# Kernel tuning notes

Hardware: AMD Instinct MI355X
Metric: run time of the kernel (lower is better)

The kernel has to match this reference:

```python
import jax, jax.numpy as jnp
import numpy as np
from jax import lax

B = 256
NUM_CLASSES = 10
IN_CAPS = 32 * 6 * 6  # 1152
IN_DIM = 8
OUT_DIM = 16
NUM_ITERS = 3


def squash(t, axis=-1):
    sq = jnp.sum(t * t, axis=axis, keepdims=True)
    return (sq / (1.0 + sq)) * t / jnp.sqrt(sq)


def conv2d(x, w, b, stride):
    y = lax.conv_general_dilated(x, w, (stride, stride), 'VALID',
                                 dimension_numbers=('NCHW', 'OIHW', 'NCHW'))
    return y + b[None, :, None, None]


def setup_inputs() -> dict:
    key = jax.random.key(0)
    ks = jax.random.split(key, 12)
    f = jnp.float32
    return {
        'x': jax.random.uniform(ks[0], (B, 1, 28, 28), dtype=f),
        'conv1_w': jax.random.normal(ks[1], (256, 1, 9, 9), dtype=f) * 0.05,
        'conv1_b': jnp.zeros((256,), dtype=f),
        'prim_w': jax.random.normal(ks[2], (IN_DIM * 32, 256, 9, 9), dtype=f) * 0.02,
        'prim_b': jnp.zeros((IN_DIM * 32,), dtype=f),
        'route_w': jax.random.normal(ks[3], (NUM_CLASSES, IN_CAPS, IN_DIM, OUT_DIM), dtype=f),
        'dec_w1': jax.random.normal(ks[4], (OUT_DIM * NUM_CLASSES, 512), dtype=f) * 0.05,
        'dec_b1': jnp.zeros((512,), dtype=f),
        'dec_w2': jax.random.normal(ks[5], (512, 1024), dtype=f) * 0.04,
        'dec_b2': jnp.zeros((1024,), dtype=f),
        'dec_w3': jax.random.normal(ks[6], (1024, 28 * 28), dtype=f) * 0.03,
        'dec_b3': jnp.zeros((28 * 28,), dtype=f),
    }


def reference(x, conv1_w, conv1_b, prim_w, prim_b, route_w,
              dec_w1, dec_b1, dec_w2, dec_b2, dec_w3, dec_b3):
    bsz = x.shape[0]
    # conv1 + relu -> [B,256,20,20]
    h = jax.nn.relu(conv2d(x, conv1_w, conv1_b, 1))
    # primary capsules: 8 parallel convs (stacked into one) -> [B, 8*32, 6, 6]
    p = conv2d(h, prim_w, prim_b, 2)
    # each capsule conv flattens to [B, 32*36], concatenated along last dim
    p = p.reshape(bsz, IN_DIM, 32 * 6 * 6).transpose(0, 2, 1)  # [B, 1152, 8]
    u = squash(p, axis=-1)
    # priors: [o, b, i, d_out]
    priors = jnp.einsum('bic,oicd->obid', u, route_w)
    # routing by agreement: softmax over in_capsules (dim i), per original code
    logits = jnp.zeros((NUM_CLASSES, bsz, IN_CAPS, 1), dtype=priors.dtype)
    outputs = None
    for it in range(NUM_ITERS):
        probs = jax.nn.softmax(logits, axis=2)              # [o,b,i,1]
        outputs = squash(jnp.sum(probs * priors, axis=2, keepdims=True))  # [o,b,1,d]
        if it != NUM_ITERS - 1:
            logits = logits + jnp.sum(priors * outputs, axis=-1, keepdims=True)
    vecs = outputs.reshape(NUM_CLASSES, bsz, OUT_DIM).transpose(1, 0, 2)  # [B,10,16]
    classes = jnp.sqrt(jnp.sum(vecs * vecs, axis=-1))
    classes = jax.nn.softmax(classes, axis=1)               # [B,10]
    # y=None path: one-hot of predicted class (non-differentiable mask)
    y = jax.nn.one_hot(jnp.argmax(classes, axis=1), NUM_CLASSES, dtype=vecs.dtype)
    dec_in = (vecs * y[:, :, None]).reshape(bsz, -1)        # [B,160]
    hdec = jax.nn.relu(dec_in @ dec_w1 + dec_b1)
    hdec = jax.nn.relu(hdec @ dec_w2 + dec_b2)
    reconstruction = jax.nn.sigmoid(hdec @ dec_w3 + dec_b3)  # [B,784]
    return classes, reconstruction
```

## Files before the change

### kernel.cpp

```cpp
#include <hip/hip_runtime.h>
#include <hip/hip_bf16.h>
#include <math.h>


typedef __attribute__((ext_vector_type(8))) short bf16x8;
typedef __attribute__((ext_vector_type(4))) float f32x4;

__device__ __forceinline__ void gl16(const void* g, void* l) {
  __builtin_amdgcn_global_load_lds((const __attribute__((address_space(1))) void*)g,
                                   (__attribute__((address_space(3))) void*)l,
                                   16, 0, 0);
}

__global__ __launch_bounds__(256) void k_conv1(const float* __restrict__ x,
                                               const float* __restrict__ w,
                                               const float* __restrict__ bias,
                                               __hip_bfloat16* __restrict__ hT) {
  const int bid = blockIdx.x;
  const int img = bid >> 2, ocq = bid & 3;
  __shared__ float xs[784];
  __shared__ float ws[64 * 81];
  __shared__ __attribute__((aligned(16))) __hip_bfloat16 tile[8 * 1288];
  const int t = threadIdx.x;
  const float4* xg = (const float4*)(x + (size_t)img * 784);
  if (t < 196) ((float4*)xs)[t] = xg[t];
  const float4* wg = (const float4*)(w + (size_t)ocq * 64 * 81);
  for (int i = t; i < 1296; i += 256) ((float4*)ws)[i] = wg[i];
  __syncthreads();
  const int ocl = t & 63, rowg = t >> 6;
  const int oc = ocq * 64 + ocl;
  const int chl = ocl >> 3, icl = ocl & 7;
  const float bv = bias[oc];
  __hip_bfloat16* hb = hT + ((size_t)img * 32 + ocq * 8) * 6560;
#pragma unroll 1
  for (int it = 0; it < 5; it++) {
    const int r = it * 4 + rowg;
    float acc[20];
#pragma unroll
    for (int p = 0; p < 20; p++) acc[p] = bv;
#pragma unroll
    for (int ky = 0; ky < 9; ky++) {
      float xr[28];
      const float* xrow = &xs[(r + ky) * 28];
#pragma unroll
      for (int q = 0; q < 7; q++) ((float4*)xr)[q] = ((const float4*)xrow)[q];
      float wr[9];
#pragma unroll
      for (int i = 0; i < 9; i++) wr[i] = ws[ocl * 81 + ky * 9 + i];
#pragma unroll
      for (int kx = 0; kx < 9; kx++)
#pragma unroll
        for (int p = 0; p < 20; p++)
          acc[p] = fmaf(wr[kx], xr[p + kx], acc[p]);
    }
#pragma unroll
    for (int p = 0; p < 20; p++) {
      const float v = fmaxf(acc[p], 0.f);
      const __hip_bfloat16 hi = __float2bfloat16(v);
      const __hip_bfloat16 lo = __float2bfloat16(v - __bfloat162float(hi));
      tile[chl * 1288 + (p * 8 + rowg * 2) * 8 + icl] = hi;
      tile[chl * 1288 + (p * 8 + rowg * 2 + 1) * 8 + icl] = lo;
    }
    __syncthreads();
#pragma unroll
    for (int q = 0; q < 5; q++) {
      const int idx = q * 256 + t;
      const int c2 = idx / 160, rem = idx - c2 * 160;
      const int xx = rem >> 3, j = rem & 7;
      const float4 vdat = *(const float4*)&tile[c2 * 1288 + rem * 8];
      *(float4*)(hb + (size_t)c2 * 6560 + (size_t)(xx * 41 + it * 8 + j) * 8) = vdat;
    }
    __syncthreads();
  }
}

__global__ __launch_bounds__(256) void k_wrep(const float* __restrict__ pw,
                                              __hip_bfloat16* __restrict__ wGp) {
  const int s = blockIdx.x >> 2, ocq = blockIdx.x & 3;
  const int ch = s / 21, tq = s - ch * 21;
  __hip_bfloat16* outp = wGp + ((size_t)s * 4 + ocq) * 4608;
  const int t = threadIdx.x;
  for (int e = t; e < 2048; e += 256) {
    const int ocl = e >> 5, k = e & 31;
    const int tapl = k >> 3, icl = k & 7;
    const int tap = tq * 4 + tapl, ic = ch * 8 + icl;
    const int oc = ocq * 64 + ocl;
    const float v = (tap < 81) ? pw[((size_t)oc * 256 + ic) * 81 + tap] : 0.f;
    const __hip_bfloat16 hi = __float2bfloat16(v);
    const __hip_bfloat16 lo = __float2bfloat16(v - __bfloat162float(hi));
    outp[ocl * 72 + k] = hi;
    outp[ocl * 72 + 32 + k] = lo;
  }
  for (int e = t; e < 512; e += 256) {
    const int ocl = e >> 3, j = e & 7;
    outp[ocl * 72 + 64 + j] = __float2bfloat16(0.f);
  }
}

__global__ __launch_bounds__(256) void k_rrep(const float* __restrict__ rw,
                                              float* __restrict__ rwT) {
  const int o = blockIdx.x / 18, ig = blockIdx.x % 18;
  __shared__ float tile[64 * 129];
  const int t = threadIdx.x;
  for (int idx = t; idx < 64 * 128; idx += 256) {
    const int i = idx >> 7, cd = idx & 127;
    tile[i * 129 + cd] = rw[((size_t)o * 1152 + ig * 64 + i) * 128 + cd];
  }
  __syncthreads();
  for (int idx = t; idx < 64 * 128; idx += 256) {
    const int cd = idx >> 6, il = idx & 63;
    rwT[((size_t)o * 128 + cd) * 1152 + ig * 64 + il] = tile[il * 129 + cd];
  }
}

#define HT_B 52480
#define PQ_F 2359296
__global__ __launch_bounds__(512) void k_conv2(
    const __hip_bfloat16* __restrict__ hTg,
    const __hip_bfloat16* __restrict__ wGp,
    float* __restrict__ pq, int c0) {
  __shared__ char hT[HT_B];
  const int bid = blockIdx.x;
  int ig, ocq, kq;
  if (gridDim.x == 512) {
    ig = (bid & 7) | (((bid >> 5) & 7) << 3);
    ocq = (bid >> 3) & 3;
    kq = bid >> 8;
  } else {
    ig = bid >> 3;
    ocq = (bid >> 1) & 3;
    kq = bid & 1;
  }
  const int t = threadIdx.x;
  const int w = t >> 6, lane = t & 63;
  const int lquad = lane >> 4, lrow = lane & 15;
  const int mhalf = w >> 2;
  const int nt = mhalf ? 4 : 5;
  const int mtb = mhalf ? 5 : 0;
  const int ocg = ocq * 64 + (w & 3) * 16 + lrow;
  int abase[5];
#pragma unroll
  for (int i = 0; i < 5; i++) {
    int m = (mtb + i) * 16 + lrow;
    if (i >= nt) m = 0;
    const int img = m / 36, px = m - img * 36;
    const int oy = px / 6, ox = px - oy * 6;
    abase[i] = img * 13120 + ox * 1312 + oy * 64;
  }
  f32x4 acc[5];
#pragma unroll
  for (int i = 0; i < 5; i++) acc[i] = (f32x4){0.f, 0.f, 0.f, 0.f};

  const char* hgc = (const char*)hTg;
  const char* wp = (const char*)wGp + ((size_t)(kq * 336) * 4 + ocq) * 4608 +
                   ((w & 3) * 16 + lrow) * 144 + lquad * 16;
  bf16x8 bh = *(const bf16x8*)wp;
  bf16x8 bl = *(const bf16x8*)(wp + 64);
  wp += 18432;
#pragma unroll 1
  for (int chl = 0; chl < 16; chl++) {
    const int ch = kq * 16 + chl;
    const char* hch = hgc + ((size_t)(ig * 128) + ch) * 13120;
#pragma unroll
    for (int rr = 0; rr < 6; rr++) {
      const int idx = t + rr * 512;
      const int j = idx / 820, r = idx - j * 820;
      gl16(hch + (size_t)j * 419840 + r * 16, hT + rr * 8192 + w * 1024);
    }
    if (t < 208) {
      const int idx = 3072 + t;
      const int j = idx / 820, r = idx - j * 820;
      gl16(hch + (size_t)j * 419840 + r * 16, hT + 49152 + w * 1024);
    }
    __syncthreads();
#pragma unroll 1
    for (int tq = 0; tq < 21; tq++) {
      const bf16x8 nh = *(const bf16x8*)wp;
      const bf16x8 nl = *(const bf16x8*)(wp + 64);
      wp += 18432;
      const int tt = tq * 4 + lquad;
      const int ky = tt / 9, kx = tt - ky * 9;
      const int toff = kx * 656 + ky * 32;
      bf16x8 ah[5];
#pragma unroll
      for (int i = 0; i < 5; i++)
        ah[i] = *(const bf16x8*)(hT + abase[i] + toff);
#pragma unroll
      for (int i = 0; i < 5; i++)
        if (i < nt) acc[i] = __builtin_amdgcn_mfma_f32_16x16x32_bf16(ah[i], bh, acc[i], 0, 0, 0);
#pragma unroll
      for (int i = 0; i < 5; i++)
        if (i < nt) acc[i] = __builtin_amdgcn_mfma_f32_16x16x32_bf16(ah[i], bl, acc[i], 0, 0, 0);
      bf16x8 al[5];
#pragma unroll
      for (int i = 0; i < 5; i++)
        al[i] = *(const bf16x8*)(hT + abase[i] + toff + 16);
#pragma unroll
      for (int i = 0; i < 5; i++)
        if (i < nt) acc[i] = __builtin_amdgcn_mfma_f32_16x16x32_bf16(al[i], bh, acc[i], 0, 0, 0);
      bh = nh;
      bl = nl;
    }
    __syncthreads();
  }
  float* pblk = pq + (size_t)kq * PQ_F;
#pragma unroll
  for (int i = 0; i < 5; i++) {
    if (i < nt) {
#pragma unroll
      for (int r = 0; r < 4; r++) {
        const int m = (mtb + i) * 16 + lquad * 4 + r;
        const int img = m / 36, px = m - img * 36;
        pblk[((size_t)(c0 + ig * 4 + img) * 36 + px) * 256 + ocg] = acc[i][r];
      }
    }
  }
}

__global__ __launch_bounds__(256) void k_squash(const float* __restrict__ pq,
                                                const float* __restrict__ bias,
                                                float* __restrict__ u) {
  const int gid = blockIdx.x * 256 + threadIdx.x;
  const int b = gid / 1152, i = gid - b * 1152;
  const int cp = i / 36, px = i - cp * 36;
  const float* pb = pq + ((size_t)b * 36 + px) * 256 + cp;
  float s[8];
#pragma unroll
  for (int d = 0; d < 8; d++)
    s[d] = pb[d * 32] + pb[(size_t)PQ_F + d * 32] + bias[cp + d * 32];
  float sq = 0.f;
#pragma unroll
  for (int d = 0; d < 8; d++) sq = fmaf(s[d], s[d], sq);
  const float scale = sq / ((1.f + sq) * sqrtf(sq));
  float o[8];
#pragma unroll
  for (int d = 0; d < 8; d++) o[d] = s[d] * scale;
  float* ub = u + (size_t)gid * 8;
  ((float4*)ub)[0] = ((float4*)o)[0];
  ((float4*)ub)[1] = ((float4*)o)[1];
}

__device__ __forceinline__ float wsum(float v) {
#pragma unroll
  for (int o = 32; o > 0; o >>= 1) v += __shfl_xor(v, o, 64);
  return v;
}
__device__ __forceinline__ float wmaxr(float v) {
#pragma unroll
  for (int o = 32; o > 0; o >>= 1) v = fmaxf(v, __shfl_xor(v, o, 64));
  return v;
}

__global__ __launch_bounds__(512) void k_route(const float* __restrict__ u,
                                               const float* __restrict__ rwT,
                                               float* __restrict__ vecs) {
  const int bid = blockIdx.x;
  int o, b;
  if (bid < 2048) { o = bid & 7; b = bid >> 3; }
  else { const int ix = bid - 2048; o = 8 + (ix & 1); b = ix >> 1; }
  __shared__ __attribute__((aligned(16))) float pri4[4 * 1152 * 4];
  __shared__ float red[8 * 17];
  __shared__ float redm[8];
  const int t = threadIdx.x;
  const int wave = t >> 6, lane = t & 63;
  const float* ub = u + (size_t)b * 9216;
  const float* rwo = rwT + (size_t)o * 128 * 1152;
#pragma unroll
  for (int ci = 0; ci < 3; ci++) {
    const bool valid = (ci < 2) || (t < 128);
    const int i = valid ? (t + ci * 512) : 0;
    float uv[8];
    *(float4*)&uv[0] = *(const float4*)(ub + i * 8);
    *(float4*)&uv[4] = *(const float4*)(ub + i * 8 + 4);
    float a[16];
#pragma unroll
    for (int d = 0; d < 16; d++) a[d] = 0.f;
#pragma unroll
    for (int c = 0; c < 8; c++) {
      const float* wcol = rwo + (size_t)(c * 16) * 1152 + i;
#pragma unroll
      for (int d = 0; d < 16; d++)
        a[d] = fmaf(uv[c], wcol[(size_t)d * 1152], a[d]);
    }
    if (valid) {
#pragma unroll
      for (int q = 0; q < 4; q++)
        *(float4*)&pri4[(q * 1152 + i) * 4] = *(float4*)&a[q * 4];
    }
  }
  __syncthreads();
  float l[3];
#pragma unroll
  for (int ci = 0; ci < 3; ci++)
    l[ci] = ((ci < 2) || (t < 128)) ? 0.f : -1e30f;
  float v[16];
#pragma unroll 1
  for (int it = 0; it < 3; it++) {
    float m = fmaxf(fmaxf(l[0], l[1]), l[2]);
    m = wmaxr(m);
    if (lane == 0) redm[wave] = m;
    __syncthreads();
    m = redm[0];
#pragma unroll
    for (int wv2 = 1; wv2 < 8; wv2++) m = fmaxf(m, redm[wv2]);
    float Z = 0.f, S[16];
#pragma unroll
    for (int d = 0; d < 16; d++) S[d] = 0.f;
#pragma unroll
    for (int ci = 0; ci < 3; ci++) {
      const bool valid = (ci < 2) || (t < 128);
      const int i = valid ? (t + ci * 512) : 0;
      const float e = expf(l[ci] - m);
      Z += e;
#pragma unroll
      for (int q = 0; q < 4; q++) {
        const float4 p4 = *(const float4*)&pri4[(q * 1152 + i) * 4];
        S[q * 4 + 0] = fmaf(e, p4.x, S[q * 4 + 0]);
        S[q * 4 + 1] = fmaf(e, p4.y, S[q * 4 + 1]);
        S[q * 4 + 2] = fmaf(e, p4.z, S[q * 4 + 2]);
        S[q * 4 + 3] = fmaf(e, p4.w, S[q * 4 + 3]);
      }
    }
    Z = wsum(Z);
#pragma unroll
    for (int d = 0; d < 16; d++) S[d] = wsum(S[d]);
    __syncthreads();
    if (lane == 0) {
      red[wave * 17] = Z;
#pragma unroll
      for (int d = 0; d < 16; d++) red[wave * 17 + 1 + d] = S[d];
    }
    __syncthreads();
    float Zt = 0.f;
#pragma unroll
    for (int wv2 = 0; wv2 < 8; wv2++) Zt += red[wv2 * 17];
    float sv[16], sq = 0.f;
#pragma unroll
    for (int d = 0; d < 16; d++) {
      float sd = 0.f;
#pragma unroll
      for (int wv2 = 0; wv2 < 8; wv2++) sd += red[wv2 * 17 + 1 + d];
      sd /= Zt;
      sv[d] = sd;
      sq = fmaf(sd, sd, sq);
    }
    const float scale = sq / ((1.f + sq) * sqrtf(sq));
#pragma unroll
    for (int d = 0; d < 16; d++) v[d] = scale * sv[d];
    if (it < 2) {
#pragma unroll
      for (int ci = 0; ci < 3; ci++) {
        const bool valid = (ci < 2) || (t < 128);
        const int i = valid ? (t + ci * 512) : 0;
        float dot = 0.f;
#pragma unroll
        for (int q = 0; q < 4; q++) {
          const float4 p4 = *(const float4*)&pri4[(q * 1152 + i) * 4];
          dot = fmaf(p4.x, v[q * 4 + 0], dot);
          dot = fmaf(p4.y, v[q * 4 + 1], dot);
          dot = fmaf(p4.z, v[q * 4 + 2], dot);
          dot = fmaf(p4.w, v[q * 4 + 3], dot);
        }
        l[ci] += dot;
      }
      __syncthreads();
    }
  }
  if (t == 0) {
    float* vb = vecs + ((size_t)b * 10 + o) * 16;
#pragma unroll
    for (int d = 0; d < 16; d++) vb[d] = v[d];
  }
}

__global__ __launch_bounds__(64) void k_cls(const float* __restrict__ vecs,
                                            float* __restrict__ out,
                                            float* __restrict__ selvec,
                                            int* __restrict__ amv) {
  const int b = blockIdx.x * 64 + threadIdx.x;
  const float* vb = vecs + (size_t)b * 160;
  float n[10];
#pragma unroll
  for (int o = 0; o < 10; o++) {
    float sq = 0.f;
#pragma unroll
    for (int d = 0; d < 16; d++) { const float xv = vb[o * 16 + d]; sq = fmaf(xv, xv, sq); }
    n[o] = sqrtf(sq);
  }
  float m = n[0];
#pragma unroll
  for (int o = 1; o < 10; o++) m = fmaxf(m, n[o]);
  float e[10], Z = 0.f;
#pragma unroll
  for (int o = 0; o < 10; o++) { e[o] = expf(n[o] - m); Z += e[o]; }
  const float inv = 1.f / Z;
  float cls[10];
#pragma unroll
  for (int o = 0; o < 10; o++) {
    cls[o] = e[o] * inv;
    out[(size_t)b * 10 + o] = cls[o];
  }
  int am = 0;
  float best = cls[0];
#pragma unroll
  for (int o = 1; o < 10; o++)
    if (cls[o] > best) { best = cls[o]; am = o; }
  amv[b] = am;
#pragma unroll
  for (int d = 0; d < 16; d++) selvec[(size_t)b * 16 + d] = vb[am * 16 + d];
}

__global__ __launch_bounds__(512) void k_dec1(const float* __restrict__ selvec,
                                              const int* __restrict__ amv,
                                              const float* __restrict__ w1,
                                              const float* __restrict__ b1,
                                              float* __restrict__ h1) {
  const int b = blockIdx.x, t = threadIdx.x;
  __shared__ float sv[16];
  __shared__ int ams;
  if (t < 16) sv[t] = selvec[(size_t)b * 16 + t];
  if (t == 0) ams = amv[b];
  __syncthreads();
  const float* wrow = w1 + (size_t)ams * 16 * 512;
  float acc = b1[t];
#pragma unroll
  for (int d = 0; d < 16; d++) acc = fmaf(sv[d], wrow[d * 512 + t], acc);
  h1[(size_t)b * 512 + t] = fmaxf(acc, 0.f);
}

__global__ __launch_bounds__(128) void k_dec2(const float* __restrict__ h1,
                                              const float* __restrict__ w2,
                                              const float* __restrict__ b2,
                                              float* __restrict__ h2) {
  const int nc = blockIdx.x >> 5, bg = blockIdx.x & 31;
  const int t = threadIdx.x;
  const int n = nc * 128 + t;
  const int bs = bg * 8;
  __shared__ float h1s[8 * 512];
  __shared__ float wts[32 * 128];
  {
    const float4* src = (const float4*)(h1 + (size_t)bs * 512);
    for (int i = t; i < 1024; i += 128) ((float4*)h1s)[i] = src[i];
  }
  float acc[8];
  const float bb = b2[n];
#pragma unroll
  for (int j = 0; j < 8; j++) acc[j] = bb;
#pragma unroll 1
  for (int kt = 0; kt < 16; kt++) {
    __syncthreads();
#pragma unroll
    for (int r = 0; r < 32; r++)
      wts[r * 128 + t] = w2[(size_t)(kt * 32 + r) * 1024 + n];
    __syncthreads();
#pragma unroll
    for (int k4 = 0; k4 < 8; k4++) {
      float wq[4];
#pragma unroll
      for (int q = 0; q < 4; q++) wq[q] = wts[(k4 * 4 + q) * 128 + t];
#pragma unroll
      for (int j = 0; j < 8; j++) {
        const float4 hv = *(const float4*)&h1s[j * 512 + kt * 32 + k4 * 4];
        acc[j] = fmaf(hv.x, wq[0], acc[j]);
        acc[j] = fmaf(hv.y, wq[1], acc[j]);
        acc[j] = fmaf(hv.z, wq[2], acc[j]);
        acc[j] = fmaf(hv.w, wq[3], acc[j]);
      }
    }
  }
#pragma unroll
  for (int j = 0; j < 8; j++) h2[(size_t)(bs + j) * 1024 + n] = fmaxf(acc[j], 0.f);
}

__global__ __launch_bounds__(128) void k_dec3(const float* __restrict__ h2,
                                              const float* __restrict__ w3,
                                              const float* __restrict__ b3,
                                              float* __restrict__ out) {
  const int nc = blockIdx.x >> 5, bg = blockIdx.x & 31;
  const int t = threadIdx.x;
  const int bs = bg * 8;
  __shared__ float h2s[8 * 1024];
  __shared__ float wts[32 * 112];
  {
    const float4* src = (const float4*)(h2 + (size_t)bs * 1024);
    for (int i = t; i < 2048; i += 128) ((float4*)h2s)[i] = src[i];
  }
  const int n = nc * 112 + (t < 112 ? t : 0);
  float acc[8];
  const float bb = b3[n];
#pragma unroll
  for (int j = 0; j < 8; j++) acc[j] = bb;
#pragma unroll 1
  for (int kt = 0; kt < 32; kt++) {
    __syncthreads();
#pragma unroll
    for (int r = 0; r < 32; r++)
      if (t < 112) wts[r * 112 + t] = w3[(size_t)(kt * 32 + r) * 784 + n];
    __syncthreads();
    if (t < 112) {
#pragma unroll
      for (int k4 = 0; k4 < 8; k4++) {
        float wq[4];
#pragma unroll
        for (int q = 0; q < 4; q++) wq[q] = wts[(k4 * 4 + q) * 112 + t];
#pragma unroll
        for (int j = 0; j < 8; j++) {
          const float4 hv = *(const float4*)&h2s[j * 1024 + kt * 32 + k4 * 4];
          acc[j] = fmaf(hv.x, wq[0], acc[j]);
          acc[j] = fmaf(hv.y, wq[1], acc[j]);
          acc[j] = fmaf(hv.z, wq[2], acc[j]);
          acc[j] = fmaf(hv.w, wq[3], acc[j]);
        }
      }
    }
  }
  if (t < 112) {
#pragma unroll
    for (int j = 0; j < 8; j++)
      out[(size_t)(bs + j) * 784 + n] = 1.f / (1.f + expf(-acc[j]));
  }
}

extern "C" void kernel_launch(void* const* d_in, const int* in_sizes, int n_in,
                              void* d_out, int out_size, void* d_ws, size_t ws_size,
                              hipStream_t stream) {
  const float* x   = (const float*)d_in[0];
  const float* c1w = (const float*)d_in[1];
  const float* c1b = (const float*)d_in[2];
  const float* pw  = (const float*)d_in[3];
  const float* pb  = (const float*)d_in[4];
  const float* rw  = (const float*)d_in[5];
  const float* w1  = (const float*)d_in[6];
  const float* b1  = (const float*)d_in[7];
  const float* w2  = (const float*)d_in[8];
  const float* b2  = (const float*)d_in[9];
  const float* w3  = (const float*)d_in[10];
  const float* b3  = (const float*)d_in[11];
  float* out = (float*)d_out;
  float* ws = (float*)d_ws;

  const size_t WGP_F = ((size_t)672 * 4 * 4608 + 18432) / 4;
  const size_t U_F = 2359296;
  const size_t RWT_F = 10 * 128 * 1152;
  const size_t SMALL_F = 40960 + 4096 + 256 + 131072 + 262144;
  const size_t fixed_f = WGP_F + 2 * PQ_F + U_F + RWT_F + SMALL_F;
  int chunk = 256;
  while (chunk > 8 && (fixed_f + (size_t)chunk * 104960) * 4 > ws_size) chunk >>= 1;

  __hip_bfloat16* wGp  = (__hip_bfloat16*)ws;
  __hip_bfloat16* hTgc = (__hip_bfloat16*)(ws + WGP_F);
  float* pq   = ws + WGP_F + (size_t)chunk * 104960;
  float* u    = pq + 2 * PQ_F;
  float* rwT  = u + U_F;
  float* vecs = rwT + RWT_F;
  float* sel  = vecs + 40960;
  int*   amv  = (int*)(sel + 4096);
  float* h1   = sel + 4096 + 256;
  float* h2   = h1 + 131072;

  k_wrep<<<dim3(2688), dim3(256), 0, stream>>>(pw, wGp);
  k_rrep<<<dim3(180), dim3(256), 0, stream>>>(rw, rwT);
  for (int c0 = 0; c0 < 256; c0 += chunk) {
    k_conv1<<<dim3(chunk * 4), dim3(256), 0, stream>>>(x + (size_t)c0 * 784, c1w, c1b, hTgc);
    k_conv2<<<dim3((chunk / 4) * 8), dim3(512), 0, stream>>>(hTgc, wGp, pq, c0);
  }
  k_squash<<<dim3(1152), dim3(256), 0, stream>>>(pq, pb, u);
  k_route<<<dim3(2560), dim3(512), 0, stream>>>(u, rwT, vecs);
  k_cls<<<dim3(4), dim3(64), 0, stream>>>(vecs, out, sel, amv);
  k_dec1<<<dim3(256), dim3(512), 0, stream>>>(sel, amv, w1, b1, h1);
  k_dec2<<<dim3(256), dim3(128), 0, stream>>>(h1, w2, b2, h2);
  k_dec3<<<dim3(224), dim3(128), 0, stream>>>(h2, w3, b3, out + 2560);
}
```

Before: 866.0 us.

## Restructure squash, classifier and decoder kernels for coalescing and more blocks

Squash now runs one block per image, staging the summed split-K partial conv outputs through padded shared memory with coalesced float4 loads instead of strided per-thread gathers. The class softmax kernel moves from one thread per image to one block per image, using shared memory for the norms. The decoder GEMM kernels process 2 images per block instead of 8, which quadruples the grid size for better CU occupancy. The cost is that each block re-reads the weight tiles four times as often, raising global weight traffic.

```diff
diff --git a/kernel.cpp b/kernel.cpp
--- a/kernel.cpp
+++ b/kernel.cpp
@@ -220,24 +220,41 @@
 __global__ __launch_bounds__(256) void k_squash(const float* __restrict__ pq,
                                                 const float* __restrict__ bias,
                                                 float* __restrict__ u) {
-  const int gid = blockIdx.x * 256 + threadIdx.x;
-  const int b = gid / 1152, i = gid - b * 1152;
-  const int cp = i / 36, px = i - cp * 36;
-  const float* pb = pq + ((size_t)b * 36 + px) * 256 + cp;
-  float s[8];
-#pragma unroll
-  for (int d = 0; d < 8; d++)
-    s[d] = pb[d * 32] + pb[(size_t)PQ_F + d * 32] + bias[cp + d * 32];
-  float sq = 0.f;
-#pragma unroll
-  for (int d = 0; d < 8; d++) sq = fmaf(s[d], s[d], sq);
-  const float scale = sq / ((1.f + sq) * sqrtf(sq));
-  float o[8];
-#pragma unroll
-  for (int d = 0; d < 8; d++) o[d] = s[d] * scale;
-  float* ub = u + (size_t)gid * 8;
-  ((float4*)ub)[0] = ((float4*)o)[0];
-  ((float4*)ub)[1] = ((float4*)o)[1];
+  const int b = blockIdx.x;
+  __shared__ float ps[36 * 257];
+  const int t = threadIdx.x;
+  const float4* s0 = (const float4*)(pq + (size_t)b * 9216);
+  const float4* s1 = (const float4*)(pq + (size_t)PQ_F + (size_t)b * 9216);
+#pragma unroll
+  for (int q = 0; q < 9; q++) {
+    const int idx = q * 256 + t;
+    const float4 a = s0[idx], c = s1[idx];
+    const int px = idx >> 6, oc = (idx & 63) * 4;
+    float* dst = &ps[px * 257 + oc];
+    dst[0] = a.x + c.x; dst[1] = a.y + c.y;
+    dst[2] = a.z + c.z; dst[3] = a.w + c.w;
+  }
+  __syncthreads();
+#pragma unroll
+  for (int rr = 0; rr < 5; rr++) {
+    const int i = rr * 256 + t;
+    if (i < 1152) {
+      const int cp = i / 36, px = i - cp * 36;
+      float s[8], sq = 0.f;
+#pragma unroll
+      for (int d = 0; d < 8; d++) {
+        s[d] = ps[px * 257 + d * 32 + cp] + bias[d * 32 + cp];
+        sq = fmaf(s[d], s[d], sq);
+      }
+      const float scale = sq / ((1.f + sq) * sqrtf(sq));
+      float o[8];
+#pragma unroll
+      for (int d = 0; d < 8; d++) o[d] = s[d] * scale;
+      float* ub = u + ((size_t)b * 1152 + i) * 8;
+      ((float4*)ub)[0] = ((float4*)o)[0];
+      ((float4*)ub)[1] = ((float4*)o)[1];
+    }
+  }
 }
 
 __device__ __forceinline__ float wsum(float v) {
@@ -377,37 +394,41 @@
                                             float* __restrict__ out,
                                             float* __restrict__ selvec,
                                             int* __restrict__ amv) {
-  const int b = blockIdx.x * 64 + threadIdx.x;
+  const int b = blockIdx.x, t = threadIdx.x;
+  __shared__ float vbs[160];
+  __shared__ float nrm[10];
+  __shared__ int ams;
   const float* vb = vecs + (size_t)b * 160;
-  float n[10];
-#pragma unroll
-  for (int o = 0; o < 10; o++) {
+  for (int idx = t; idx < 160; idx += 64) vbs[idx] = vb[idx];
+  __syncthreads();
+  if (t < 10) {
     float sq = 0.f;
 #pragma unroll
-    for (int d = 0; d < 16; d++) { const float xv = vb[o * 16 + d]; sq = fmaf(xv, xv, sq); }
-    n[o] = sqrtf(sq);
-  }
-  float m = n[0];
-#pragma unroll
-  for (int o = 1; o < 10; o++) m = fmaxf(m, n[o]);
-  float e[10], Z = 0.f;
-#pragma unroll
-  for (int o = 0; o < 10; o++) { e[o] = expf(n[o] - m); Z += e[o]; }
-  const float inv = 1.f / Z;
-  float cls[10];
-#pragma unroll
-  for (int o = 0; o < 10; o++) {
-    cls[o] = e[o] * inv;
-    out[(size_t)b * 10 + o] = cls[o];
-  }
-  int am = 0;
-  float best = cls[0];
-#pragma unroll
-  for (int o = 1; o < 10; o++)
-    if (cls[o] > best) { best = cls[o]; am = o; }
-  amv[b] = am;
-#pragma unroll
-  for (int d = 0; d < 16; d++) selvec[(size_t)b * 16 + d] = vb[am * 16 + d];
+    for (int d = 0; d < 16; d++) { const float xv = vbs[t * 16 + d]; sq = fmaf(xv, xv, sq); }
+    nrm[t] = sqrtf(sq);
+  }
+  __syncthreads();
+  if (t == 0) {
+    float m = nrm[0];
+#pragma unroll
+    for (int o = 1; o < 10; o++) m = fmaxf(m, nrm[o]);
+    float e[10], Z = 0.f;
+#pragma unroll
+    for (int o = 0; o < 10; o++) { e[o] = expf(nrm[o] - m); Z += e[o]; }
+    const float inv = 1.f / Z;
+    int am = 0;
+    float best = e[0] * inv;
+#pragma unroll
+    for (int o = 0; o < 10; o++) {
+      const float c = e[o] * inv;
+      out[(size_t)b * 10 + o] = c;
+      if (o > 0 && c > best) { best = c; am = o; }
+    }
+    amv[b] = am;
+    ams = am;
+  }
+  __syncthreads();
+  if (t < 16) selvec[(size_t)b * 16 + t] = vbs[ams * 16 + t];
 }
 
 __global__ __launch_bounds__(512) void k_dec1(const float* __restrict__ selvec,
@@ -432,20 +453,19 @@
                                               const float* __restrict__ w2,
                                               const float* __restrict__ b2,
                                               float* __restrict__ h2) {
-  const int nc = blockIdx.x >> 5, bg = blockIdx.x & 31;
+  const int nc = blockIdx.x >> 7, bg = blockIdx.x & 127;
   const int t = threadIdx.x;
   const int n = nc * 128 + t;
-  const int bs = bg * 8;
-  __shared__ float h1s[8 * 512];
+  const int bs = bg * 2;
+  __shared__ float h1s[2 * 512];
   __shared__ float wts[32 * 128];
   {
     const float4* src = (const float4*)(h1 + (size_t)bs * 512);
-    for (int i = t; i < 1024; i += 128) ((float4*)h1s)[i] = src[i];
-  }
-  float acc[8];
+    for (int i = t; i < 256; i += 128) ((float4*)h1s)[i] = src[i];
+  }
+  float acc[2];
   const float bb = b2[n];
-#pragma unroll
-  for (int j = 0; j < 8; j++) acc[j] = bb;
+  acc[0] = bb; acc[1] = bb;
 #pragma unroll 1
   for (int kt = 0; kt < 16; kt++) {
     __syncthreads();
@@ -459,7 +479,7 @@
 #pragma unroll
       for (int q = 0; q < 4; q++) wq[q] = wts[(k4 * 4 + q) * 128 + t];
 #pragma unroll
-      for (int j = 0; j < 8; j++) {
+      for (int j = 0; j < 2; j++) {
         const float4 hv = *(const float4*)&h1s[j * 512 + kt * 32 + k4 * 4];
         acc[j] = fmaf(hv.x, wq[0], acc[j]);
         acc[j] = fmaf(hv.y, wq[1], acc[j]);
@@ -469,27 +489,26 @@
     }
   }
 #pragma unroll
-  for (int j = 0; j < 8; j++) h2[(size_t)(bs + j) * 1024 + n] = fmaxf(acc[j], 0.f);
+  for (int j = 0; j < 2; j++) h2[(size_t)(bs + j) * 1024 + n] = fmaxf(acc[j], 0.f);
 }
 
 __global__ __launch_bounds__(128) void k_dec3(const float* __restrict__ h2,
                                               const float* __restrict__ w3,
                                               const float* __restrict__ b3,
                                               float* __restrict__ out) {
-  const int nc = blockIdx.x >> 5, bg = blockIdx.x & 31;
-  const int t = threadIdx.x;
-  const int bs = bg * 8;
-  __shared__ float h2s[8 * 1024];
+  const int nc = blockIdx.x >> 7, bg = blockIdx.x & 127;
+  const int t = threadIdx.x;
+  const int bs = bg * 2;
+  __shared__ float h2s[2 * 1024];
   __shared__ float wts[32 * 112];
   {
     const float4* src = (const float4*)(h2 + (size_t)bs * 1024);
-    for (int i = t; i < 2048; i += 128) ((float4*)h2s)[i] = src[i];
+    for (int i = t; i < 512; i += 128) ((float4*)h2s)[i] = src[i];
   }
   const int n = nc * 112 + (t < 112 ? t : 0);
-  float acc[8];
+  float acc[2];
   const float bb = b3[n];
-#pragma unroll
-  for (int j = 0; j < 8; j++) acc[j] = bb;
+  acc[0] = bb; acc[1] = bb;
 #pragma unroll 1
   for (int kt = 0; kt < 32; kt++) {
     __syncthreads();
@@ -504,7 +523,7 @@
 #pragma unroll
         for (int q = 0; q < 4; q++) wq[q] = wts[(k4 * 4 + q) * 112 + t];
 #pragma unroll
-        for (int j = 0; j < 8; j++) {
+        for (int j = 0; j < 2; j++) {
           const float4 hv = *(const float4*)&h2s[j * 1024 + kt * 32 + k4 * 4];
           acc[j] = fmaf(hv.x, wq[0], acc[j]);
           acc[j] = fmaf(hv.y, wq[1], acc[j]);
@@ -516,7 +535,7 @@
   }
   if (t < 112) {
 #pragma unroll
-    for (int j = 0; j < 8; j++)
+    for (int j = 0; j < 2; j++)
       out[(size_t)(bs + j) * 784 + n] = 1.f / (1.f + expf(-acc[j]));
   }
 }
@@ -564,10 +583,10 @@
     k_conv1<<<dim3(chunk * 4), dim3(256), 0, stream>>>(x + (size_t)c0 * 784, c1w, c1b, hTgc);
     k_conv2<<<dim3((chunk / 4) * 8), dim3(512), 0, stream>>>(hTgc, wGp, pq, c0);
   }
-  k_squash<<<dim3(1152), dim3(256), 0, stream>>>(pq, pb, u);
+  k_squash<<<dim3(256), dim3(256), 0, stream>>>(pq, pb, u);
   k_route<<<dim3(2560), dim3(512), 0, stream>>>(u, rwT, vecs);
-  k_cls<<<dim3(4), dim3(64), 0, stream>>>(vecs, out, sel, amv);
+  k_cls<<<dim3(256), dim3(64), 0, stream>>>(vecs, out, sel, amv);
   k_dec1<<<dim3(256), dim3(512), 0, stream>>>(sel, amv, w1, b1, h1);
-  k_dec2<<<dim3(256), dim3(128), 0, stream>>>(h1, w2, b2, h2);
-  k_dec3<<<dim3(224), dim3(128), 0, stream>>>(h2, w3, b3, out + 2560);
-}
+  k_dec2<<<dim3(1024), dim3(128), 0, stream>>>(h1, w2, b2, h2);
+  k_dec3<<<dim3(896), dim3(128), 0, stream>>>(h2, w3, b3, out + 2560);
+}
```

New measurement: 808.9 us. 6.6% less time.
